# Kernel optimization log

Measured on AMD Instinct MI355X. Metric: run time of the kernel, lower is better.

The kernel has to match this reference:

```python
import jax, jax.numpy as jnp
import numpy as np

B, T, CM, CZ, H = 2, 512, 256, 128, 16
DH = CM // H  # 16
EPS = 1e-5


def setup_inputs() -> dict:
    root = jax.random.key(0)
    ks = jax.random.split(root, 16)
    n = lambda i, shape: jax.random.normal(ks[i], shape, dtype=jnp.float32)
    s = np.float32(1.0 / np.sqrt(CM))
    return dict(
        query=n(0, (B, T, CM)),
        key=n(1, (B, T, CM)),
        value=n(2, (B, T, CM)),
        pos_embedding=n(3, (B, 2 * T - 1, CM)),  # T2 = 2T-1 relative positions
        z=n(4, (B, T, T, CZ)),
        mask=jax.random.randint(ks[5], (B, 1, T), 0, 2) > 0,
        Wq=n(6, (CM, CM)) * s, bq=jnp.zeros((CM,), jnp.float32),
        Wk=n(7, (CM, CM)) * s, bk=jnp.zeros((CM,), jnp.float32),
        Wv=n(8, (CM, CM)) * s, bv=jnp.zeros((CM,), jnp.float32),
        Wp=n(9, (CM, CM)) * s,
        u_bias=n(10, (H, DH)) * np.float32(0.1),
        v_bias=n(11, (H, DH)) * np.float32(0.1),
        Wo=n(12, (CM, CM)) * s, bo=jnp.zeros((CM,), jnp.float32),
        ln_g=jnp.ones((CZ,), jnp.float32), ln_b=jnp.zeros((CZ,), jnp.float32),
        Wz=n(13, (CZ, H)) * np.float32(1.0 / np.sqrt(CZ)),
    )


def _relative_shift(ps):
    # ps: (B, H, T1, T2) -> Transformer-XL relative shift, keep first T2//2+1 cols
    b, h, t1, t2 = ps.shape
    padded = jnp.pad(ps, ((0, 0), (0, 0), (0, 0), (1, 0)))  # (b,h,t1,t2+1)
    padded = padded.reshape(b, h, t2 + 1, t1)
    shifted = padded[:, :, 1:, :].reshape(b, h, t1, t2)
    return shifted[..., : t2 // 2 + 1]


def reference(query, key, value, pos_embedding, z, mask,
              Wq, bq, Wk, bk, Wv, bv, Wp, u_bias, v_bias, Wo, bo,
              ln_g, ln_b, Wz):
    b = query.shape[0]
    q = (query @ Wq.T + bq).reshape(b, -1, H, DH)          # (b,T,H,dh)
    k = (key @ Wk.T + bk).reshape(b, -1, H, DH)
    v = (value @ Wv.T + bv).reshape(b, -1, H, DH)
    p = (pos_embedding @ Wp.T).reshape(b, -1, H, DH)       # (b,2T-1,H,dh)

    content = jnp.einsum('bihd,bjhd->bhij', q + u_bias, k)     # (b,H,T,T)
    pos = jnp.einsum('bihd,bjhd->bhij', q + v_bias, p)         # (b,H,T,2T-1)
    pos = _relative_shift(pos)                                  # (b,H,T,T)

    # z bias: LayerNorm over c_z then project to heads (chunking in torch is a no-op math-wise)
    mu = jnp.mean(z, axis=-1, keepdims=True)
    var = jnp.var(z, axis=-1, keepdims=True)
    zn = (z - mu) * jax.lax.rsqrt(var + EPS) * ln_g + ln_b
    z_bias = jnp.einsum('bijc,ch->bhij', zn, Wz)                # (b,H,T,T)

    score = (content + pos) / np.float32(np.sqrt(DH)) + z_bias
    score = jnp.where(mask[:, None, :, :], jnp.float32(-10000.0), score)
    attn = jax.nn.softmax(score, axis=-1)  # dropout is identity in eval

    ctx = jnp.einsum('bhij,bjhd->bihd', attn, v).reshape(b, -1, CM)
    return ctx @ Wo.T + bo
```

## Files before the change

### kernel.cpp

```cpp
#include <hip/hip_runtime.h>
#include <hip/hip_bf16.h>

typedef __attribute__((ext_vector_type(8))) short short8;
typedef __attribute__((ext_vector_type(4))) short short4v;
typedef __attribute__((ext_vector_type(4))) float f32x4;

#define LD4(dst, v4) { dst[0]=(v4).x; dst[1]=(v4).y; dst[2]=(v4).z; dst[3]=(v4).w; }

static __device__ __forceinline__ short f2bf(float f) {
    union { float f; unsigned u; } v; v.f = f;
    unsigned r = (v.u + 0x7FFFu + ((v.u >> 16) & 1u)) >> 16;
    return (short)r;
}
static __device__ __forceinline__ float bf2f(short s) {
    union { unsigned u; float f; } v; v.u = ((unsigned)(unsigned short)s) << 16;
    return v.f;
}
static __device__ __forceinline__ unsigned cvt_pk_bf16(float lo, float hi) {
    unsigned r;
    asm volatile("v_cvt_pk_bf16_f32 %0, %1, %2" : "=v"(r) : "v"(lo), "v"(hi));
    return r;
}

static __device__ __forceinline__ void proj_tile(
    const float* __restrict__ X, const float* __restrict__ W,
    const float* __restrict__ bias, float* __restrict__ Yf,
    short* __restrict__ Yb, int M, int base, float* xs)
{
    int rt = base >> 1, ct = base & 1;
    int t = threadIdx.x;
    int row_base = rt * 32;
    {
        int r = t >> 3, k0 = (t & 7) * 32;
        int row = row_base + r;
        if (row < M) {
            const float* xp = X + (size_t)row * 256 + k0;
            #pragma unroll
            for (int q = 0; q < 8; ++q) {
                float4 v = *(const float4*)(xp + q * 4);
                xs[(k0 + q * 4 + 0) * 36 + r] = v.x;
                xs[(k0 + q * 4 + 1) * 36 + r] = v.y;
                xs[(k0 + q * 4 + 2) * 36 + r] = v.z;
                xs[(k0 + q * 4 + 3) * 36 + r] = v.w;
            }
        } else {
            #pragma unroll
            for (int q = 0; q < 32; ++q) xs[(k0 + q) * 36 + r] = 0.f;
        }
    }
    __syncthreads();
    int c_base = ct * 128 + (t & 31) * 4;
    int r_base = (t >> 5) * 4;
    float acc[4][4];
    #pragma unroll
    for (int a = 0; a < 4; ++a)
        #pragma unroll
        for (int b = 0; b < 4; ++b) acc[a][b] = 0.f;
    for (int k = 0; k < 256; k += 4) {
        float w0[4], w1[4], w2[4], w3[4];
        { float4 v = *(const float4*)(W + (size_t)(c_base + 0) * 256 + k); LD4(w0, v); }
        { float4 v = *(const float4*)(W + (size_t)(c_base + 1) * 256 + k); LD4(w1, v); }
        { float4 v = *(const float4*)(W + (size_t)(c_base + 2) * 256 + k); LD4(w2, v); }
        { float4 v = *(const float4*)(W + (size_t)(c_base + 3) * 256 + k); LD4(w3, v); }
        #pragma unroll
        for (int kk = 0; kk < 4; ++kk) {
            float xl[4];
            float4 xv = *(const float4*)(&xs[(k + kk) * 36 + r_base]);
            LD4(xl, xv);
            #pragma unroll
            for (int ri = 0; ri < 4; ++ri) {
                acc[ri][0] += xl[ri] * w0[kk];
                acc[ri][1] += xl[ri] * w1[kk];
                acc[ri][2] += xl[ri] * w2[kk];
                acc[ri][3] += xl[ri] * w3[kk];
            }
        }
    }
    #pragma unroll
    for (int ri = 0; ri < 4; ++ri) {
        int row = row_base + r_base + ri;
        if (row < M) {
            float o0 = acc[ri][0] + (bias ? bias[c_base + 0] : 0.f);
            float o1 = acc[ri][1] + (bias ? bias[c_base + 1] : 0.f);
            float o2 = acc[ri][2] + (bias ? bias[c_base + 2] : 0.f);
            float o3 = acc[ri][3] + (bias ? bias[c_base + 3] : 0.f);
            if (Yb) {
                short4v o; o[0] = f2bf(o0); o[1] = f2bf(o1); o[2] = f2bf(o2); o[3] = f2bf(o3);
                *(short4v*)(Yb + (size_t)row * 256 + c_base) = o;
            } else {
                float4 o; o.x = o0; o.y = o1; o.z = o2; o.w = o3;
                *(float4*)(Yf + (size_t)row * 256 + c_base) = o;
            }
        }
    }
}

__global__ void k_proj(const float* __restrict__ query, const float* __restrict__ key,
                       const float* __restrict__ value, const float* __restrict__ pos,
                       const float* __restrict__ Wq, const float* __restrict__ bq,
                       const float* __restrict__ Wk, const float* __restrict__ bk,
                       const float* __restrict__ Wv, const float* __restrict__ bv,
                       const float* __restrict__ Wp,
                       const float* __restrict__ ln_g, const float* __restrict__ ln_b,
                       const float* __restrict__ Wz, const int* __restrict__ mask,
                       float* __restrict__ qb, short* __restrict__ kbf,
                       short* __restrict__ vbf, short* __restrict__ pbf,
                       short* __restrict__ wzp, float* __restrict__ Ah, float* __restrict__ Ch,
                       int* __restrict__ idx, int* __restrict__ cnt)
{
    __shared__ float xs[256 * 36];
    int bx = blockIdx.x;
    if (bx == 320) {
        int lane = threadIdx.x & 63, wave = threadIdx.x >> 6;
        if (wave == 0) {
            for (int b = 0; b < 2; ++b) {
                int* idxb = idx + b * 512;
                #pragma unroll
                for (int q = 0; q < 8; ++q) idxb[q * 64 + lane] = -1;
                int total = 0;
                for (int q = 0; q < 8; ++q) {
                    int j = q * 64 + lane;
                    int u = (mask[b * 512 + j] == 0) ? 1 : 0;
                    unsigned long long bal = __ballot(u);
                    int p = total + __popcll(bal & ((1ull << lane) - 1ull));
                    if (u) idxb[p] = j;
                    total += (int)__popcll(bal);
                }
                if (total == 0) {
                    for (int q = 0; q < 8; ++q) idxb[q * 64 + lane] = q * 64 + lane;
                    total = 512;
                }
                if (lane == 0) cnt[b] = total;
            }
        } else if (wave == 1) {
            for (int id = lane; id < 2048; id += 64) {
                int m = id >> 9, rem = id & 511, l = rem >> 3, ii = rem & 7;
                int c = m * 32 + ((l >> 4) << 3) + ii, h = l & 15;
                wzp[id] = f2bf(ln_g[c] * Wz[c * 16 + h]);
            }
        } else if (wave == 2) {
            int h = lane & 15, part = lane >> 4;
            float a = 0.f, c = 0.f;
            #pragma unroll 4
            for (int cc = part * 32; cc < part * 32 + 32; ++cc) {
                float wv = Wz[cc * 16 + h];
                a += ln_g[cc] * wv;
                c += ln_b[cc] * wv;
            }
            a += __shfl_xor(a, 16); a += __shfl_xor(a, 32);
            c += __shfl_xor(c, 16); c += __shfl_xor(c, 32);
            if (part == 0) { Ah[h] = a; Ch[h] = c; }
        }
        return;
    }
    if (bx < 64)       proj_tile(query, Wq, bq, qb, nullptr, 1024, bx, xs);
    else if (bx < 128) proj_tile(key,   Wk, bk, nullptr, kbf, 1024, bx - 64, xs);
    else if (bx < 192) proj_tile(value, Wv, bv, nullptr, vbf, 1024, bx - 128, xs);
    else               proj_tile(pos,   Wp, nullptr, nullptr, pbf, 2046, bx - 192, xs);
}

__global__ void __launch_bounds__(256, 4) k_z(
    const float* __restrict__ z, const short* __restrict__ wzp,
    const float* __restrict__ Ah, const float* __restrict__ Ch,
    const int* __restrict__ idx, const int* __restrict__ cnt,
    const short* __restrict__ kbf, const short* __restrict__ vbf,
    short* __restrict__ kbfC, short* __restrict__ vbTC, short* __restrict__ zacc)
{
    __shared__ short ldsb[8448];
    int bx = blockIdx.x;
    const short8 z8v = {0,0,0,0,0,0,0,0};
    if (bx < 32) {
        short* st = ldsb;
        int b = bx >> 4, jn0 = (bx & 15) * 32;
        int t = threadIdx.x;
        int r = t >> 3, cc = (t & 7) * 32;
        int jn = jn0 + r;
        int jv = idx[b * 512 + jn];
        {
            short* dst = kbfC + ((size_t)b * 512 + jn) * 256 + cc;
            if (jv >= 0) {
                const short* src = kbf + ((size_t)b * 512 + jv) * 256 + cc;
                #pragma unroll
                for (int q = 0; q < 4; ++q) *(short8*)(dst + q * 8) = *(const short8*)(src + q * 8);
            } else {
                #pragma unroll
                for (int q = 0; q < 4; ++q) *(short8*)(dst + q * 8) = z8v;
            }
        }
        {
            if (jv >= 0) {
                const short* src = vbf + ((size_t)b * 512 + jv) * 256 + cc;
                #pragma unroll
                for (int q = 0; q < 4; ++q) *(short8*)(&st[r * 264 + cc + q * 8]) = *(const short8*)(src + q * 8);
            } else {
                #pragma unroll
                for (int q = 0; q < 4; ++q) *(short8*)(&st[r * 264 + cc + q * 8]) = z8v;
            }
            __syncthreads();
            int c = t;
            short tmp[32];
            #pragma unroll
            for (int q = 0; q < 32; ++q) tmp[q] = st[q * 264 + c];
            short* dst = vbTC + ((size_t)b * 256 + c) * 512 + jn0;
            #pragma unroll
            for (int q = 0; q < 4; ++q) *(short8*)(dst + q * 8) = *(const short8*)(&tmp[q * 8]);
        }
        return;
    }
    int wave = threadIdx.x >> 6, lane = threadIdx.x & 63;
    int w = (bx - 32) * 4 + wave;
    int bi = w >> 5, tl = w & 31;
    int b = bi >> 9;
    int np = (min(cnt[b], 512) + 31) & ~31;
    if (tl * 16 >= np) return;
    short* zs = ldsb + wave * 2112;
    const int* idxr = idx + b * 512 + tl * 16;
    const float* zb_ = z + (size_t)bi * 65536;
    int l5 = lane >> 5, l31 = lane & 31;
    int idxv = idxr[lane & 15];
    #pragma unroll
    for (int m = 0; m < 8; ++m) {
        int r = 2 * m + l5;
        int jv = __shfl(idxv, r);
        int jr = (jv < 0) ? 0 : jv;
        float4 v = *(const float4*)(zb_ + (size_t)jr * 128 + l31 * 4);
        uint2 pk;
        pk.x = cvt_pk_bf16(v.x, v.y);
        pk.y = cvt_pk_bf16(v.z, v.w);
        *(uint2*)(&zs[r * 132 + l31 * 4]) = pk;
    }
    int h = lane & 15, g = lane >> 4;
    short8 wz[4];
    #pragma unroll
    for (int m = 0; m < 4; ++m) wz[m] = *(const short8*)(wzp + m * 512 + lane * 8);
    short8 af[4];
    float sum = 0.f, sq = 0.f;
    #pragma unroll
    for (int m = 0; m < 4; ++m) {
        short4v a0 = *(const short4v*)(&zs[h * 132 + g * 8 + m * 32]);
        short4v a1 = *(const short4v*)(&zs[h * 132 + g * 8 + m * 32 + 4]);
        short8 s8;
        s8[0] = a0[0]; s8[1] = a0[1]; s8[2] = a0[2]; s8[3] = a0[3];
        s8[4] = a1[0]; s8[5] = a1[1]; s8[6] = a1[2]; s8[7] = a1[3];
        af[m] = s8;
        #pragma unroll
        for (int ii = 0; ii < 8; ++ii) {
            float x = bf2f(s8[ii]);
            sum += x;
            sq = fmaf(x, x, sq);
        }
    }
    sum += __shfl_xor(sum, 16); sum += __shfl_xor(sum, 32);
    sq  += __shfl_xor(sq, 16);  sq  += __shfl_xor(sq, 32);
    float mu = sum * (1.f / 128.f);
    float rs = rsqrtf(sq * (1.f / 128.f) - mu * mu + 1e-5f);
    f32x4 acc = {0.f, 0.f, 0.f, 0.f};
    #pragma unroll
    for (int m = 0; m < 4; ++m)
        acc = __builtin_amdgcn_mfma_f32_16x16x32_bf16(af[m], wz[m], acc, 0, 0, 0);
    float ah = Ah[h], ch = Ch[h];
    short4v o;
    #pragma unroll
    for (int reg = 0; reg < 4; ++reg) {
        int orow = g * 4 + reg;
        float mo = __shfl(mu, orow);
        float ro = __shfl(rs, orow);
        o[reg] = f2bf(ro * (acc[reg] - mo * ah) + ch);
    }
    *(short4v*)(zacc + ((size_t)bi * 16 + h) * 512 + tl * 16 + g * 4) = o;
}

__global__ void __launch_bounds__(256, 4) k_attn4(
    const float* __restrict__ qb, const short* __restrict__ kbfC, const short* __restrict__ pbf,
    const short* __restrict__ zacc,
    const float* __restrict__ u_bias, const float* __restrict__ v_bias,
    const int* __restrict__ idx, const int* __restrict__ cnt,
    const short* __restrict__ vbTC,
    const float* __restrict__ Wo, const float* __restrict__ bo, float* __restrict__ out)
{
    __shared__ short wT[16 * 520];
    __shared__ float redm[64], reds[64];
    __shared__ float ctx_lds[256];
    const short8 zero8 = {0, 0, 0, 0, 0, 0, 0, 0};

    int bi = blockIdx.x;
    int b = bi >> 9, i = bi & 511;
    int t = threadIdx.x;
    int lane = t & 63, wave = t >> 6;
    int h = lane & 15, g = lane >> 4;
    int np = (min(cnt[b], 512) + 31) & ~31;
    int nt16 = np >> 4;

    bool act = ((h & 1) == (g >> 1));
    int m_act = act ? (h >> 1) : 8;
    short8 qu8 = zero8, qv8 = zero8;
    {
        int c0q = h * 16 + (g & 1) * 8;
        const float* qp = qb + (size_t)bi * 256 + c0q;
        #pragma unroll
        for (int ii = 0; ii < 8; ++ii) {
            float qv_ = qp[ii];
            qu8[ii] = f2bf(0.25f * (qv_ + u_bias[c0q + ii]));
            qv8[ii] = f2bf(0.25f * (qv_ + v_bias[c0q + ii]));
        }
        if (!act) { qu8 = zero8; qv8 = zero8; }
    }

    f32x4 sc[8];
    float mloc = -3.0e38f;
    #pragma unroll
    for (int q = 0; q < 8; ++q) {
        int tl = wave + q * 4;
        if (tl < nt16) {
            int jn = tl * 16 + h;
            int jvh = idx[b * 512 + jn];
            int jrp = 511 + ((jvh < 0) ? 0 : jvh) - i;
            const short* kr = kbfC + ((size_t)b * 512 + jn) * 256 + g * 8;
            const short* pr = pbf + ((size_t)b * 1023 + jrp) * 256 + g * 8;
            f32x4 acp = {0.f, 0.f, 0.f, 0.f};
            #pragma unroll
            for (int m = 0; m < 8; ++m) {
                short8 ka = *(const short8*)(kr + m * 32);
                short8 pa = *(const short8*)(pr + m * 32);
                short8 bu = (m == m_act) ? qu8 : zero8;
                short8 bv = (m == m_act) ? qv8 : zero8;
                acp = __builtin_amdgcn_mfma_f32_16x16x32_bf16(ka, bu, acp, 0, 0, 0);
                acp = __builtin_amdgcn_mfma_f32_16x16x32_bf16(pa, bv, acp, 0, 0, 0);
            }
            short4v za = *(const short4v*)(zacc + ((size_t)bi * 16 + h) * 512 + tl * 16 + g * 4);
            int4 jv4 = *(const int4*)(idx + b * 512 + tl * 16 + g * 4);
            int jj4[4]; jj4[0] = jv4.x; jj4[1] = jv4.y; jj4[2] = jv4.z; jj4[3] = jv4.w;
            #pragma unroll
            for (int reg = 0; reg < 4; ++reg) {
                float s = acp[reg] + bf2f(za[reg]);
                s = (jj4[reg] < 0) ? -3.0e38f : s;
                sc[q][reg] = s;
                mloc = fmaxf(mloc, s);
            }
        }
    }

    mloc = fmaxf(mloc, __shfl_xor(mloc, 16));
    mloc = fmaxf(mloc, __shfl_xor(mloc, 32));
    redm[wave * 16 + h] = mloc;
    __syncthreads();
    float mg = fmaxf(fmaxf(redm[h], redm[16 + h]), fmaxf(redm[32 + h], redm[48 + h]));
    float ssum = 0.f;
    #pragma unroll
    for (int q = 0; q < 8; ++q) {
        int tl = wave + q * 4;
        if (tl < nt16) {
            #pragma unroll
            for (int reg = 0; reg < 4; ++reg) {
                float e = __expf(sc[q][reg] - mg);
                sc[q][reg] = e;
                ssum += e;
            }
        }
    }
    ssum += __shfl_xor(ssum, 16); ssum += __shfl_xor(ssum, 32);
    reds[wave * 16 + h] = ssum;
    __syncthreads();
    float sg = reds[h] + reds[16 + h] + reds[32 + h] + reds[48 + h];
    float inv = 1.f / sg;
    #pragma unroll
    for (int q = 0; q < 8; ++q) {
        int tl = wave + q * 4;
        if (tl < nt16) {
            short4v w4;
            #pragma unroll
            for (int reg = 0; reg < 4; ++reg) w4[reg] = f2bf(sc[q][reg] * inv);
            *(short4v*)(&wT[h * 520 + tl * 16 + g * 4]) = w4;
        }
    }
    __syncthreads();

    #pragma unroll
    for (int q = 0; q < 4; ++q) {
        int hp = wave * 4 + q;
        int c0 = hp * 16;
        const short* vrow = vbTC + ((size_t)b * 256 + c0 + h) * 512;
        f32x4 a0 = {0.f, 0.f, 0.f, 0.f};
        for (int jn0 = 0; jn0 < np; jn0 += 32) {
            short8 wA = *(const short8*)(&wT[hp * 520 + jn0 + g * 8]);
            short8 vB = *(const short8*)(vrow + jn0 + g * 8);
            a0 = __builtin_amdgcn_mfma_f32_16x16x32_bf16(wA, vB, a0, 0, 0, 0);
        }
        if (g == 0) ctx_lds[c0 + h] = a0[0];
    }
    __syncthreads();

    {
        float acc = bo[t];
        const float* wrow = Wo + (size_t)t * 256;
        #pragma unroll 4
        for (int k = 0; k < 256; k += 8) {
            float4 w0 = *(const float4*)(wrow + k);
            float4 w1 = *(const float4*)(wrow + k + 4);
            acc += ctx_lds[k + 0] * w0.x + ctx_lds[k + 1] * w0.y
                 + ctx_lds[k + 2] * w0.z + ctx_lds[k + 3] * w0.w
                 + ctx_lds[k + 4] * w1.x + ctx_lds[k + 5] * w1.y
                 + ctx_lds[k + 6] * w1.z + ctx_lds[k + 7] * w1.w;
        }
        out[(size_t)bi * 256 + t] = acc;
    }
}

extern "C" void kernel_launch(void* const* d_in, const int* in_sizes, int n_in,
                              void* d_out, int out_size, void* d_ws, size_t ws_size,
                              hipStream_t stream) {
    const float* query = (const float*)d_in[0];
    const float* key   = (const float*)d_in[1];
    const float* value = (const float*)d_in[2];
    const float* pos   = (const float*)d_in[3];
    const float* z     = (const float*)d_in[4];
    const int*   mask  = (const int*)d_in[5];
    const float* Wq = (const float*)d_in[6];
    const float* bq = (const float*)d_in[7];
    const float* Wk = (const float*)d_in[8];
    const float* bk = (const float*)d_in[9];
    const float* Wv = (const float*)d_in[10];
    const float* bv = (const float*)d_in[11];
    const float* Wp = (const float*)d_in[12];
    const float* u_bias = (const float*)d_in[13];
    const float* v_bias = (const float*)d_in[14];
    const float* Wo = (const float*)d_in[15];
    const float* bo = (const float*)d_in[16];
    const float* ln_g = (const float*)d_in[17];
    const float* ln_b = (const float*)d_in[18];
    const float* Wz = (const float*)d_in[19];

    char* ws = (char*)d_ws;
    float* qb   = (float*)(ws + 0);
    short* kbf  = (short*)(ws + (1u << 20));
    short* vbf  = (short*)(ws + 1572864u);
    short* pbf  = (short*)(ws + (2u << 20));
    short* wzp  = (short*)(ws + (3u << 20));
    float* Ah   = (float*)(ws + (3u << 20) + 4096);
    float* Ch   = (float*)(ws + (3u << 20) + 4160);
    int*   idx  = (int*)(ws + (3u << 20) + 8192);
    int*   cnt  = (int*)(ws + (3u << 20) + 16384);
    short* kbfC = (short*)(ws + (4u << 20));
    short* vbTC = (short*)(ws + 4718592u);
    short* zacc = (short*)(ws + (5u << 20));

    hipLaunchKernelGGL(k_proj, dim3(321), dim3(256), 0, stream,
                       query, key, value, pos, Wq, bq, Wk, bk, Wv, bv, Wp,
                       ln_g, ln_b, Wz, mask,
                       qb, kbf, vbf, pbf, wzp, Ah, Ch, idx, cnt);
    hipLaunchKernelGGL(k_z, dim3(8224), dim3(256), 0, stream,
                       z, wzp, Ah, Ch, idx, cnt, kbf, vbf, kbfC, vbTC, zacc);
    hipLaunchKernelGGL(k_attn4, dim3(1024), dim3(256), 0, stream,
                       qb, kbfC, pbf, zacc, u_bias, v_bias, idx, cnt, vbTC,
                       Wo, bo, (float*)d_out);
}
```

Measured before the change: 183.9 us.

## Fuse z LayerNorm-projection bias into attention kernel, split out compaction kernel

Moves the per-row z LayerNorm plus Wz projection (bf16 MFMA) into the attention kernel, so each attention block loads its z rows itself and builds the bias in registers. This removes the zacc workspace write and re-read and the large 8224-block launch. The K/V compaction and transpose now runs as its own small 32-block kernel. In exchange the attention kernel uses more LDS (about 35 KB) and more registers, with launch bounds lowered to 3 blocks per CU, and the z loads now sit inside the score loop.

```diff
diff --git a/kernel.cpp b/kernel.cpp
--- a/kernel.cpp
+++ b/kernel.cpp
@@ -159,128 +159,64 @@
     else               proj_tile(pos,   Wp, nullptr, nullptr, pbf, 2046, bx - 192, xs);
 }
 
-__global__ void __launch_bounds__(256, 4) k_z(
-    const float* __restrict__ z, const short* __restrict__ wzp,
-    const float* __restrict__ Ah, const float* __restrict__ Ch,
-    const int* __restrict__ idx, const int* __restrict__ cnt,
-    const short* __restrict__ kbf, const short* __restrict__ vbf,
-    short* __restrict__ kbfC, short* __restrict__ vbTC, short* __restrict__ zacc)
+__global__ void k_compact(const int* __restrict__ idx,
+                          const short* __restrict__ kbf, const short* __restrict__ vbf,
+                          short* __restrict__ kbfC, short* __restrict__ vbTC)
 {
-    __shared__ short ldsb[8448];
+    __shared__ short st[32 * 264];
+    const short8 z8v = {0,0,0,0,0,0,0,0};
     int bx = blockIdx.x;
-    const short8 z8v = {0,0,0,0,0,0,0,0};
-    if (bx < 32) {
-        short* st = ldsb;
-        int b = bx >> 4, jn0 = (bx & 15) * 32;
-        int t = threadIdx.x;
-        int r = t >> 3, cc = (t & 7) * 32;
-        int jn = jn0 + r;
-        int jv = idx[b * 512 + jn];
-        {
-            short* dst = kbfC + ((size_t)b * 512 + jn) * 256 + cc;
-            if (jv >= 0) {
-                const short* src = kbf + ((size_t)b * 512 + jv) * 256 + cc;
-                #pragma unroll
-                for (int q = 0; q < 4; ++q) *(short8*)(dst + q * 8) = *(const short8*)(src + q * 8);
-            } else {
-                #pragma unroll
-                for (int q = 0; q < 4; ++q) *(short8*)(dst + q * 8) = z8v;
-            }
-        }
-        {
-            if (jv >= 0) {
-                const short* src = vbf + ((size_t)b * 512 + jv) * 256 + cc;
-                #pragma unroll
-                for (int q = 0; q < 4; ++q) *(short8*)(&st[r * 264 + cc + q * 8]) = *(const short8*)(src + q * 8);
-            } else {
-                #pragma unroll
-                for (int q = 0; q < 4; ++q) *(short8*)(&st[r * 264 + cc + q * 8]) = z8v;
-            }
-            __syncthreads();
-            int c = t;
-            short tmp[32];
-            #pragma unroll
-            for (int q = 0; q < 32; ++q) tmp[q] = st[q * 264 + c];
-            short* dst = vbTC + ((size_t)b * 256 + c) * 512 + jn0;
-            #pragma unroll
-            for (int q = 0; q < 4; ++q) *(short8*)(dst + q * 8) = *(const short8*)(&tmp[q * 8]);
-        }
-        return;
-    }
-    int wave = threadIdx.x >> 6, lane = threadIdx.x & 63;
-    int w = (bx - 32) * 4 + wave;
-    int bi = w >> 5, tl = w & 31;
-    int b = bi >> 9;
-    int np = (min(cnt[b], 512) + 31) & ~31;
-    if (tl * 16 >= np) return;
-    short* zs = ldsb + wave * 2112;
-    const int* idxr = idx + b * 512 + tl * 16;
-    const float* zb_ = z + (size_t)bi * 65536;
-    int l5 = lane >> 5, l31 = lane & 31;
-    int idxv = idxr[lane & 15];
-    #pragma unroll
-    for (int m = 0; m < 8; ++m) {
-        int r = 2 * m + l5;
-        int jv = __shfl(idxv, r);
-        int jr = (jv < 0) ? 0 : jv;
-        float4 v = *(const float4*)(zb_ + (size_t)jr * 128 + l31 * 4);
-        uint2 pk;
-        pk.x = cvt_pk_bf16(v.x, v.y);
-        pk.y = cvt_pk_bf16(v.z, v.w);
-        *(uint2*)(&zs[r * 132 + l31 * 4]) = pk;
-    }
-    int h = lane & 15, g = lane >> 4;
-    short8 wz[4];
-    #pragma unroll
-    for (int m = 0; m < 4; ++m) wz[m] = *(const short8*)(wzp + m * 512 + lane * 8);
-    short8 af[4];
-    float sum = 0.f, sq = 0.f;
-    #pragma unroll
-    for (int m = 0; m < 4; ++m) {
-        short4v a0 = *(const short4v*)(&zs[h * 132 + g * 8 + m * 32]);
-        short4v a1 = *(const short4v*)(&zs[h * 132 + g * 8 + m * 32 + 4]);
-        short8 s8;
-        s8[0] = a0[0]; s8[1] = a0[1]; s8[2] = a0[2]; s8[3] = a0[3];
-        s8[4] = a1[0]; s8[5] = a1[1]; s8[6] = a1[2]; s8[7] = a1[3];
-        af[m] = s8;
+    int b = bx >> 4, jn0 = (bx & 15) * 32;
+    int t = threadIdx.x;
+    int r = t >> 3, cc = (t & 7) * 32;
+    int jn = jn0 + r;
+    int jv = idx[b * 512 + jn];
+    {
+        short* dst = kbfC + ((size_t)b * 512 + jn) * 256 + cc;
+        if (jv >= 0) {
+            const short* src = kbf + ((size_t)b * 512 + jv) * 256 + cc;
+            #pragma unroll
+            for (int q = 0; q < 4; ++q) *(short8*)(dst + q * 8) = *(const short8*)(src + q * 8);
+        } else {
+            #pragma unroll
+            for (int q = 0; q < 4; ++q) *(short8*)(dst + q * 8) = z8v;
+        }
+    }
+    {
+        if (jv >= 0) {
+            const short* src = vbf + ((size_t)b * 512 + jv) * 256 + cc;
+            #pragma unroll
+            for (int q = 0; q < 4; ++q) *(short8*)(&st[r * 264 + cc + q * 8]) = *(const short8*)(src + q * 8);
+        } else {
+            #pragma unroll
+            for (int q = 0; q < 4; ++q) *(short8*)(&st[r * 264 + cc + q * 8]) = z8v;
+        }
+        __syncthreads();
+        int c = t;
+        short tmp[32];
         #pragma unroll
-        for (int ii = 0; ii < 8; ++ii) {
-            float x = bf2f(s8[ii]);
-            sum += x;
-            sq = fmaf(x, x, sq);
-        }
-    }
-    sum += __shfl_xor(sum, 16); sum += __shfl_xor(sum, 32);
-    sq  += __shfl_xor(sq, 16);  sq  += __shfl_xor(sq, 32);
-    float mu = sum * (1.f / 128.f);
-    float rs = rsqrtf(sq * (1.f / 128.f) - mu * mu + 1e-5f);
-    f32x4 acc = {0.f, 0.f, 0.f, 0.f};
-    #pragma unroll
-    for (int m = 0; m < 4; ++m)
-        acc = __builtin_amdgcn_mfma_f32_16x16x32_bf16(af[m], wz[m], acc, 0, 0, 0);
-    float ah = Ah[h], ch = Ch[h];
-    short4v o;
-    #pragma unroll
-    for (int reg = 0; reg < 4; ++reg) {
-        int orow = g * 4 + reg;
-        float mo = __shfl(mu, orow);
-        float ro = __shfl(rs, orow);
-        o[reg] = f2bf(ro * (acc[reg] - mo * ah) + ch);
-    }
-    *(short4v*)(zacc + ((size_t)bi * 16 + h) * 512 + tl * 16 + g * 4) = o;
-}
-
-__global__ void __launch_bounds__(256, 4) k_attn4(
+        for (int q = 0; q < 32; ++q) tmp[q] = st[q * 264 + c];
+        short* dst = vbTC + ((size_t)b * 256 + c) * 512 + jn0;
+        #pragma unroll
+        for (int q = 0; q < 4; ++q) *(short8*)(dst + q * 8) = *(const short8*)(&tmp[q * 8]);
+    }
+}
+
+__global__ void __launch_bounds__(256, 3) k_attn_z(
+    const float* __restrict__ z,
     const float* __restrict__ qb, const short* __restrict__ kbfC, const short* __restrict__ pbf,
-    const short* __restrict__ zacc,
+    const short* __restrict__ wzp, const float* __restrict__ Ah, const float* __restrict__ Ch,
     const float* __restrict__ u_bias, const float* __restrict__ v_bias,
     const int* __restrict__ idx, const int* __restrict__ cnt,
     const short* __restrict__ vbTC,
     const float* __restrict__ Wo, const float* __restrict__ bo, float* __restrict__ out)
 {
-    __shared__ short wT[16 * 520];
-    __shared__ float redm[64], reds[64];
-    __shared__ float ctx_lds[256];
+    __shared__ __align__(16) char lds_raw[35072];
+    short* zs_all = (short*)lds_raw;
+    short* wT   = (short*)(lds_raw + 16896);
+    float* redm = (float*)(lds_raw + 33536);
+    float* reds = (float*)(lds_raw + 33792);
+    float* ctxl = (float*)(lds_raw + 34048);
     const short8 zero8 = {0, 0, 0, 0, 0, 0, 0, 0};
 
     int bi = blockIdx.x;
@@ -288,8 +224,16 @@
     int t = threadIdx.x;
     int lane = t & 63, wave = t >> 6;
     int h = lane & 15, g = lane >> 4;
+    int l5 = lane >> 5, l31 = lane & 31;
     int np = (min(cnt[b], 512) + 31) & ~31;
     int nt16 = np >> 4;
+    short* zs = zs_all + wave * 2112;
+    const float* zb_ = z + (size_t)bi * 65536;
+
+    short8 wz[4];
+    #pragma unroll
+    for (int m = 0; m < 4; ++m) wz[m] = *(const short8*)(wzp + m * 512 + lane * 8);
+    float ah = Ah[h], ch = Ch[h];
 
     bool act = ((h & 1) == (g >> 1));
     int m_act = act ? (h >> 1) : 8;
@@ -306,14 +250,29 @@
         if (!act) { qu8 = zero8; qv8 = zero8; }
     }
 
+    int idxq[8];
+    #pragma unroll
+    for (int q = 0; q < 8; ++q) {
+        int tl = wave + q * 4;
+        idxq[q] = (tl < nt16) ? idx[b * 512 + tl * 16 + h] : -1;
+    }
+
     f32x4 sc[8];
     float mloc = -3.0e38f;
     #pragma unroll
     for (int q = 0; q < 8; ++q) {
         int tl = wave + q * 4;
         if (tl < nt16) {
+            float4 zv[8];
+            #pragma unroll
+            for (int m = 0; m < 8; ++m) {
+                int r = 2 * m + l5;
+                int jv = __shfl(idxq[q], r);
+                int jr = (jv < 0) ? 0 : jv;
+                zv[m] = *(const float4*)(zb_ + (size_t)jr * 128 + l31 * 4);
+            }
             int jn = tl * 16 + h;
-            int jvh = idx[b * 512 + jn];
+            int jvh = idxq[q];
             int jrp = 511 + ((jvh < 0) ? 0 : jvh) - i;
             const short* kr = kbfC + ((size_t)b * 512 + jn) * 256 + g * 8;
             const short* pr = pbf + ((size_t)b * 1023 + jrp) * 256 + g * 8;
@@ -327,12 +286,47 @@
                 acp = __builtin_amdgcn_mfma_f32_16x16x32_bf16(ka, bu, acp, 0, 0, 0);
                 acp = __builtin_amdgcn_mfma_f32_16x16x32_bf16(pa, bv, acp, 0, 0, 0);
             }
-            short4v za = *(const short4v*)(zacc + ((size_t)bi * 16 + h) * 512 + tl * 16 + g * 4);
+            #pragma unroll
+            for (int m = 0; m < 8; ++m) {
+                int r = 2 * m + l5;
+                uint2 pk;
+                pk.x = cvt_pk_bf16(zv[m].x, zv[m].y);
+                pk.y = cvt_pk_bf16(zv[m].z, zv[m].w);
+                *(uint2*)(&zs[r * 132 + l31 * 4]) = pk;
+            }
+            short8 af[4];
+            float sum = 0.f, sq = 0.f;
+            #pragma unroll
+            for (int m = 0; m < 4; ++m) {
+                short4v a0 = *(const short4v*)(&zs[h * 132 + g * 8 + m * 32]);
+                short4v a1 = *(const short4v*)(&zs[h * 132 + g * 8 + m * 32 + 4]);
+                short8 s8;
+                s8[0] = a0[0]; s8[1] = a0[1]; s8[2] = a0[2]; s8[3] = a0[3];
+                s8[4] = a1[0]; s8[5] = a1[1]; s8[6] = a1[2]; s8[7] = a1[3];
+                af[m] = s8;
+                #pragma unroll
+                for (int ii = 0; ii < 8; ++ii) {
+                    float x = bf2f(s8[ii]);
+                    sum += x;
+                    sq = fmaf(x, x, sq);
+                }
+            }
+            sum += __shfl_xor(sum, 16); sum += __shfl_xor(sum, 32);
+            sq  += __shfl_xor(sq, 16);  sq  += __shfl_xor(sq, 32);
+            float mu = sum * (1.f / 128.f);
+            float rs = rsqrtf(sq * (1.f / 128.f) - mu * mu + 1e-5f);
+            f32x4 accz = {0.f, 0.f, 0.f, 0.f};
+            #pragma unroll
+            for (int m = 0; m < 4; ++m)
+                accz = __builtin_amdgcn_mfma_f32_16x16x32_bf16(af[m], wz[m], accz, 0, 0, 0);
             int4 jv4 = *(const int4*)(idx + b * 512 + tl * 16 + g * 4);
             int jj4[4]; jj4[0] = jv4.x; jj4[1] = jv4.y; jj4[2] = jv4.z; jj4[3] = jv4.w;
             #pragma unroll
             for (int reg = 0; reg < 4; ++reg) {
-                float s = acp[reg] + bf2f(za[reg]);
+                int orow = g * 4 + reg;
+                float mo = __shfl(mu, orow);
+                float ro = __shfl(rs, orow);
+                float s = acp[reg] + ro * (accz[reg] - mo * ah) + ch;
                 s = (jj4[reg] < 0) ? -3.0e38f : s;
                 sc[q][reg] = s;
                 mloc = fmaxf(mloc, s);
@@ -386,7 +380,7 @@
             short8 vB = *(const short8*)(vrow + jn0 + g * 8);
             a0 = __builtin_amdgcn_mfma_f32_16x16x32_bf16(wA, vB, a0, 0, 0, 0);
         }
-        if (g == 0) ctx_lds[c0 + h] = a0[0];
+        if (g == 0) ctxl[c0 + h] = a0[0];
     }
     __syncthreads();
 
@@ -397,10 +391,10 @@
         for (int k = 0; k < 256; k += 8) {
             float4 w0 = *(const float4*)(wrow + k);
             float4 w1 = *(const float4*)(wrow + k + 4);
-            acc += ctx_lds[k + 0] * w0.x + ctx_lds[k + 1] * w0.y
-                 + ctx_lds[k + 2] * w0.z + ctx_lds[k + 3] * w0.w
-                 + ctx_lds[k + 4] * w1.x + ctx_lds[k + 5] * w1.y
-                 + ctx_lds[k + 6] * w1.z + ctx_lds[k + 7] * w1.w;
+            acc += ctxl[k + 0] * w0.x + ctxl[k + 1] * w0.y
+                 + ctxl[k + 2] * w0.z + ctxl[k + 3] * w0.w
+                 + ctxl[k + 4] * w1.x + ctxl[k + 5] * w1.y
+                 + ctxl[k + 6] * w1.z + ctxl[k + 7] * w1.w;
         }
         out[(size_t)bi * 256 + t] = acc;
     }
@@ -442,15 +436,14 @@
     int*   cnt  = (int*)(ws + (3u << 20) + 16384);
     short* kbfC = (short*)(ws + (4u << 20));
     short* vbTC = (short*)(ws + 4718592u);
-    short* zacc = (short*)(ws + (5u << 20));
 
     hipLaunchKernelGGL(k_proj, dim3(321), dim3(256), 0, stream,
                        query, key, value, pos, Wq, bq, Wk, bk, Wv, bv, Wp,
                        ln_g, ln_b, Wz, mask,
                        qb, kbf, vbf, pbf, wzp, Ah, Ch, idx, cnt);
-    hipLaunchKernelGGL(k_z, dim3(8224), dim3(256), 0, stream,
-                       z, wzp, Ah, Ch, idx, cnt, kbf, vbf, kbfC, vbTC, zacc);
-    hipLaunchKernelGGL(k_attn4, dim3(1024), dim3(256), 0, stream,
-                       qb, kbfC, pbf, zacc, u_bias, v_bias, idx, cnt, vbTC,
+    hipLaunchKernelGGL(k_compact, dim3(32), dim3(256), 0, stream,
+                       idx, kbf, vbf, kbfC, vbTC);
+    hipLaunchKernelGGL(k_attn_z, dim3(1024), dim3(256), 0, stream,
+                       z, qb, kbfC, pbf, wzp, Ah, Ch, u_bias, v_bias, idx, cnt, vbTC,
                        Wo, bo, (float*)d_out);
 }
```

After: 179.6 us. 2.3% less time.
